# Optimization experiments

Measured on AMD Instinct MI355X. Metric: run time of the kernel, lower is better.

## Reference

```python
import jax, jax.numpy as jnp
import numpy as np

N_NODES = 50000
N_EDGES = 800000
D = 64  # node_dim == edge_dim
NEG_SLOPE = 0.2
EPS = 1e-5


def _lin_params(key, d_in, d_out):
    k1, k2 = jax.random.split(key)
    bound = 1.0 / np.sqrt(d_in)
    W = jax.random.uniform(k1, (d_out, d_in), minval=-bound, maxval=bound, dtype=jnp.float32)
    b = jax.random.uniform(k2, (d_out,), minval=-bound, maxval=bound, dtype=jnp.float32)
    return W, b


def setup_inputs() -> dict:
    key = jax.random.key(0)
    ks = jax.random.split(key, 12)
    V = jax.random.normal(ks[0], (N_NODES, D), dtype=jnp.float32)
    E = jax.random.normal(ks[1], (N_EDGES, D), dtype=jnp.float32)
    src = jax.random.randint(ks[2], (N_EDGES,), 0, N_NODES, dtype=jnp.int32)
    dst = jax.random.randint(ks[3], (N_EDGES,), 0, N_NODES, dtype=jnp.int32)
    pA_w, pA_b = _lin_params(ks[4], D, D)   # NodePooling.A
    pB_w, pB_b = _lin_params(ks[5], D, D)   # NodePooling.B
    mW1, mb1 = _lin_params(ks[6], D, D)     # edge MLP layer 1
    mW2, mb2 = _lin_params(ks[7], D, D)     # edge MLP layer 2
    BW, Bb = _lin_params(ks[8], D, D)       # GenMessage.B (scale)
    CW, Cb = _lin_params(ks[9], D, D)       # GenMessage.C (shift)
    return {"V": V, "E": E, "src": src, "dst": dst,
            "pA_w": pA_w, "pA_b": pA_b, "pB_w": pB_w, "pB_b": pB_b,
            "mW1": mW1, "mb1": mb1, "mW2": mW2, "mb2": mb2,
            "BW": BW, "Bb": Bb, "CW": CW, "Cb": Cb}


def _lrelu(x):
    return jnp.where(x >= 0, x, NEG_SLOPE * x)


def reference(V, E, src, dst, pA_w, pA_b, pB_w, pB_b, mW1, mb1, mW2, mb2, BW, Bb, CW, Cb):
    n = V.shape[0]
    # V = act(V); NodePooling: B(lrelu(A(V)))
    Va = _lrelu(V)
    Vp = _lrelu(Va @ pA_w.T + pA_b) @ pB_w.T + pB_b  # [N, D]
    # edge MLP on edge features (2 Linear+ReLU layers)
    x = jax.nn.relu(E @ mW1.T + mb1)
    x = jax.nn.relu(x @ mW2.T + mb2)                  # [E, D]
    scale = jax.nn.sigmoid(x @ BW.T + Bb)
    shift = x @ CW.T + Cb
    # gathered src features, gated affine message
    M1 = scale * Vp[src] + shift                      # [E, D]
    M2 = M1 * M1
    # segment-mean onto dst (DGL fn.mean); zero for isolated nodes
    deg = jax.ops.segment_sum(jnp.ones((dst.shape[0],), jnp.float32), dst, num_segments=n)
    denom = jnp.maximum(deg, 1.0)[:, None]
    V1 = jax.ops.segment_sum(M1, dst, num_segments=n) / denom
    V2 = jax.ops.segment_sum(M2, dst, num_segments=n) / denom
    return jnp.sqrt(jax.nn.relu(V2 - V1) + EPS)
```

## Files before the change

kernel.cpp:

```cpp
#include <hip/hip_runtime.h>

#define NN 50000
#define NE 800000
#define DDIM 64
#define PADX 68
#define PADS 68
#define NB_SCAN ((NN + 255) / 256)
#define NEG_SLOPE 0.2f
#define EPS_V 1e-5f

typedef short bf16x8 __attribute__((ext_vector_type(8)));
typedef float f32x4 __attribute__((ext_vector_type(4)));

__device__ __forceinline__ float lrelu_f(float x) { return x >= 0.0f ? x : NEG_SLOPE * x; }

__device__ __forceinline__ unsigned short bf16_rn(float x) {
    union { float f; unsigned int u; } c; c.f = x;
    unsigned int r = c.u + 0x7FFF + ((c.u >> 16) & 1);
    return (unsigned short)(r >> 16);
}
__device__ __forceinline__ float bf16_tof(unsigned short h) {
    union { float f; unsigned int u; } c; c.u = ((unsigned int)h) << 16;
    return c.f;
}

__device__ __forceinline__ unsigned cvtpk_bf16(float a, float b) {
    unsigned r;
    asm("v_cvt_pk_bf16_f32 %0, %1, %2" : "=v"(r) : "v"(a), "v"(b));
    return r;
}

__device__ __forceinline__ void split8(const float* __restrict__ v, bf16x8& h, bf16x8& l)
{
    union { bf16x8 v8; unsigned u[4]; } H, L;
    #pragma unroll
    for (int k = 0; k < 4; ++k) {
        float a = v[2*k], b = v[2*k+1];
        unsigned p = cvtpk_bf16(a, b);
        union { float f; unsigned u; } h0, h1;
        h0.u = p << 16;
        h1.u = p & 0xFFFF0000u;
        unsigned q = cvtpk_bf16(a - h0.f, b - h1.f);
        H.u[k] = p;
        L.u[k] = q;
    }
    h = H.v8; l = L.v8;
}

__device__ __forceinline__ void mma_tile(float acc[16], const float* __restrict__ XT,
                                         const float* __restrict__ Wc, int e0, int f0)
{
    #pragma unroll 4
    for (int kk = 0; kk < DDIM; kk += 4) {
        float4 A0 = *(const float4*)&XT[(kk+0)*PADX + e0];
        float4 A1 = *(const float4*)&XT[(kk+1)*PADX + e0];
        float4 A2 = *(const float4*)&XT[(kk+2)*PADX + e0];
        float4 A3 = *(const float4*)&XT[(kk+3)*PADX + e0];
        float4 B0 = *(const float4*)&Wc[(f0+0)*PADX + kk];
        float4 B1 = *(const float4*)&Wc[(f0+1)*PADX + kk];
        float4 B2 = *(const float4*)&Wc[(f0+2)*PADX + kk];
        float4 B3 = *(const float4*)&Wc[(f0+3)*PADX + kk];
        const float a[4][4] = {{A0.x,A0.y,A0.z,A0.w},{A1.x,A1.y,A1.z,A1.w},
                               {A2.x,A2.y,A2.z,A2.w},{A3.x,A3.y,A3.z,A3.w}};
        const float b[4][4] = {{B0.x,B0.y,B0.z,B0.w},{B1.x,B1.y,B1.z,B1.w},
                               {B2.x,B2.y,B2.z,B2.w},{B3.x,B3.y,B3.z,B3.w}};
        #pragma unroll
        for (int j = 0; j < 4; ++j)
            #pragma unroll
            for (int i = 0; i < 4; ++i)
                #pragma unroll
                for (int q = 0; q < 4; ++q)
                    acc[i*4+j] = fmaf(a[q][i], b[j][q], acc[i*4+j]);
    }
}

__device__ __forceinline__ void load_w_f32(float* __restrict__ Wc, const float* __restrict__ Wg, int tid)
{
    #pragma unroll
    for (int c = 0; c < 4; ++c) {
        int idx = (c << 10) + (tid << 2);
        int f = idx >> 6, k = idx & 63;
        *(float4*)&Wc[f*PADX + k] = *(const float4*)&Wg[idx];
    }
}

__global__ __launch_bounds__(256, 3)
void node_pool_kernel(const float* __restrict__ V,
                      const float* __restrict__ Aw, const float* __restrict__ Ab,
                      const float* __restrict__ Bw, const float* __restrict__ Bbv,
                      float* __restrict__ Vp,
                      const int* __restrict__ dst, int* __restrict__ degi)
{
    __shared__ float Wc[DDIM*PADX];
    __shared__ float XT[DDIM*PADX];
    const int tid = threadIdx.x;
    const int nb = blockIdx.x * 64;
    const int e0 = (tid & 15) << 2;
    const int f0 = (tid >> 4) << 2;

    #pragma unroll
    for (int c = 0; c < 4; ++c) {
        int idx = (c << 10) + (tid << 2);
        int e = idx >> 6, d = idx & 63;
        int row = nb + e; if (row > NN-1) row = NN-1;
        float4 v = *(const float4*)&V[(size_t)row*DDIM + d];
        XT[(d+0)*PADX + e] = lrelu_f(v.x);
        XT[(d+1)*PADX + e] = lrelu_f(v.y);
        XT[(d+2)*PADX + e] = lrelu_f(v.z);
        XT[(d+3)*PADX + e] = lrelu_f(v.w);
    }
    load_w_f32(Wc, Aw, tid);
    __syncthreads();

    float acc[16];
    #pragma unroll
    for (int i = 0; i < 16; ++i) acc[i] = 0.f;
    mma_tile(acc, XT, Wc, e0, f0);
    __syncthreads();

    {
        float4 bv = *(const float4*)&Ab[f0];
        const float ba[4] = {bv.x, bv.y, bv.z, bv.w};
        #pragma unroll
        for (int j = 0; j < 4; ++j) {
            float4 v;
            v.x = lrelu_f(acc[0*4+j] + ba[j]);
            v.y = lrelu_f(acc[1*4+j] + ba[j]);
            v.z = lrelu_f(acc[2*4+j] + ba[j]);
            v.w = lrelu_f(acc[3*4+j] + ba[j]);
            *(float4*)&XT[(f0+j)*PADX + e0] = v;
        }
    }
    load_w_f32(Wc, Bw, tid);
    __syncthreads();

    float acc2[16];
    #pragma unroll
    for (int i = 0; i < 16; ++i) acc2[i] = 0.f;
    mma_tile(acc2, XT, Wc, e0, f0);

    float4 bv = *(const float4*)&Bbv[f0];
    #pragma unroll
    for (int i = 0; i < 4; ++i) {
        int row = nb + e0 + i;
        if (row < NN) {
            float4 o;
            o.x = acc2[i*4+0] + bv.x;
            o.y = acc2[i*4+1] + bv.y;
            o.z = acc2[i*4+2] + bv.z;
            o.w = acc2[i*4+3] + bv.w;
            *(float4*)&Vp[(size_t)row*DDIM + f0] = o;
        }
    }

    const int stride = gridDim.x * 256;
    for (int e = blockIdx.x * 256 + tid; e < NE; e += stride)
        atomicAdd(&degi[dst[e]], 1);
}

__global__ __launch_bounds__(256)
void prep_w_kernel(const float* __restrict__ W1, const float* __restrict__ W2,
                   const float* __restrict__ WB, const float* __restrict__ WC,
                   short* __restrict__ WF)
{
    int gid = blockIdx.x * 256 + threadIdx.x;
    int L = gid >> 12, r = gid & 4095;
    int t = r >> 10, ks = (r >> 9) & 1, lane = (r >> 3) & 63, j = r & 7;
    const float* Ws = (L == 0) ? W1 : (L == 1) ? W2 : (L == 2) ? WB : WC;
    int n = lane & 15, kg = lane >> 4;
    int f = t*16 + n, k = ks*32 + kg*8 + j;
    float v = Ws[f*64 + k];
    unsigned short h = bf16_rn(v);
    unsigned short l = bf16_rn(v - bf16_tof(h));
    int base = L*8192 + ((t*2 + ks)*2)*512 + lane*8 + j;
    WF[base]       = (short)h;
    WF[base + 512] = (short)l;
}

__global__ __launch_bounds__(256)
void scan1_kernel(const int* __restrict__ degi, int* __restrict__ linc, int* __restrict__ bsum)
{
    __shared__ int ws[4];
    const int tid = threadIdx.x;
    const int lane = tid & 63, wv = tid >> 6;
    int i = blockIdx.x * 256 + tid;
    int v = (i < NN) ? degi[i] : 0;
    int sc = v;
    #pragma unroll
    for (int off = 1; off < 64; off <<= 1) {
        int t = __shfl_up(sc, off, 64);
        if (lane >= off) sc += t;
    }
    if (lane == 63) ws[wv] = sc;
    __syncthreads();
    int wb = 0;
    #pragma unroll
    for (int w = 0; w < 4; ++w) if (w < wv) wb += ws[w];
    int incl = sc + wb;
    if (i < NN) linc[i] = incl;
    if (tid == 255) bsum[blockIdx.x] = incl;
}

__global__ __launch_bounds__(256)
void scan23_kernel(const int* __restrict__ degi, const int* __restrict__ linc,
                   const int* __restrict__ bsum, int* __restrict__ curs)
{
    __shared__ int ws[4];
    __shared__ int base_s;
    const int tid = threadIdx.x;
    const int lane = tid & 63, wv = tid >> 6;
    int v = (tid < NB_SCAN) ? bsum[tid] : 0;
    int sc = v;
    #pragma unroll
    for (int off = 1; off < 64; off <<= 1) {
        int t = __shfl_up(sc, off, 64);
        if (lane >= off) sc += t;
    }
    if (lane == 63) ws[wv] = sc;
    __syncthreads();
    int wb = 0;
    #pragma unroll
    for (int w = 0; w < 4; ++w) if (w < wv) wb += ws[w];
    if (tid == blockIdx.x) base_s = sc + wb - v;
    __syncthreads();
    int i = blockIdx.x * 256 + tid;
    if (i < NN) curs[i] = base_s + linc[i] - degi[i];
}

__global__ __launch_bounds__(256)
void scatter_kernel(const int* __restrict__ dst, int* __restrict__ cursor, int* __restrict__ pinv)
{
    int e = blockIdx.x * 256 + threadIdx.x;
    if (e < NE) {
        pinv[e] = atomicAdd(&cursor[dst[e]], 1);
    }
}

__device__ __forceinline__ void gemm64_dual_lds(const short* bw, int lane,
                                                const bf16x8 ah0[2], const bf16x8 al0[2],
                                                const bf16x8 ah1[2], const bf16x8 al1[2],
                                                f32x4 acc0[4], f32x4 acc1[4])
{
    #pragma unroll
    for (int ks = 0; ks < 2; ++ks) {
        bf16x8 bh[4], bl[4];
        #pragma unroll
        for (int t = 0; t < 4; ++t) {
            bh[t] = *(const bf16x8*)&bw[(((t*2 + ks)*2 + 0)*64 + lane)*8];
            bl[t] = *(const bf16x8*)&bw[(((t*2 + ks)*2 + 1)*64 + lane)*8];
        }
        #pragma unroll
        for (int t = 0; t < 4; ++t) {
            acc0[t] = __builtin_amdgcn_mfma_f32_16x16x32_bf16(al0[ks], bh[t], acc0[t], 0, 0, 0);
            acc1[t] = __builtin_amdgcn_mfma_f32_16x16x32_bf16(al1[ks], bh[t], acc1[t], 0, 0, 0);
            acc0[t] = __builtin_amdgcn_mfma_f32_16x16x32_bf16(ah0[ks], bl[t], acc0[t], 0, 0, 0);
            acc1[t] = __builtin_amdgcn_mfma_f32_16x16x32_bf16(ah1[ks], bl[t], acc1[t], 0, 0, 0);
            acc0[t] = __builtin_amdgcn_mfma_f32_16x16x32_bf16(ah0[ks], bh[t], acc0[t], 0, 0, 0);
            acc1[t] = __builtin_amdgcn_mfma_f32_16x16x32_bf16(ah1[ks], bh[t], acc1[t], 0, 0, 0);
        }
    }
}

__device__ __forceinline__ void transpose_frags(float* __restrict__ sw, const f32x4 y[4],
                                                int lane, bf16x8 ah[2], bf16x8 al[2])
{
    const int n = lane & 15, mg = lane >> 4;
    #pragma unroll
    for (int t = 0; t < 4; ++t)
        #pragma unroll
        for (int r = 0; r < 4; ++r)
            sw[(mg*4 + r)*PADS + t*16 + n] = y[t][r];
    __builtin_amdgcn_wave_barrier();
    const int m = lane & 15, kg = lane >> 4;
    float x[16];
    *(float4*)&x[0]  = *(const float4*)&sw[m*PADS + kg*8];
    *(float4*)&x[4]  = *(const float4*)&sw[m*PADS + kg*8 + 4];
    *(float4*)&x[8]  = *(const float4*)&sw[m*PADS + 32 + kg*8];
    *(float4*)&x[12] = *(const float4*)&sw[m*PADS + 32 + kg*8 + 4];
    split8(&x[0], ah[0], al[0]);
    split8(&x[8], ah[1], al[1]);
    __builtin_amdgcn_wave_barrier();
}

__global__ __launch_bounds__(256, 3)
void e1_mlp_kernel(const float* __restrict__ Eg,
                   const int* __restrict__ src, const int* __restrict__ pinv,
                   const short* __restrict__ WF,
                   const float* __restrict__ b1, const float* __restrict__ b2,
                   const float* __restrict__ bB, const float* __restrict__ bC,
                   const float* __restrict__ Vp,
                   float* __restrict__ M1s)
{
    __shared__ short bw[8192];
    __shared__ float scratch[4 * 16 * PADS];
    __shared__ int aux[4 * 64];

    const int tid = threadIdx.x;
    const int lane = tid & 63, wv = tid >> 6;
    float* sw = scratch + wv * 16 * PADS;
    int* auxw = aux + wv * 64;

    const int e0 = blockIdx.x * 128 + wv * 32;
    const int m = lane & 15, kg = lane >> 4;
    const int n = lane & 15, mg = lane >> 4;

    auto load_layer = [&](const short* Wg) {
        __syncthreads();
        const uint4* s = (const uint4*)Wg;
        uint4* d = (uint4*)bw;
        #pragma unroll
        for (int c = 0; c < 4; ++c)
            d[c*256 + tid] = s[c*256 + tid];
        __syncthreads();
    };

    if (lane < 32) {
        auxw[lane]      = pinv[e0 + lane];
        auxw[32 + lane] = src[e0 + lane];
    }
    bf16x8 ah0[2], al0[2], ah1[2], al1[2];
    {
        const float* er0 = Eg + (size_t)(e0 + m)*DDIM + kg*8;
        const float* er1 = Eg + (size_t)(e0 + 16 + m)*DDIM + kg*8;
        float x[16];
        *(float4*)&x[0]  = *(const float4*)&er0[0];
        *(float4*)&x[4]  = *(const float4*)&er0[4];
        *(float4*)&x[8]  = *(const float4*)&er0[32];
        *(float4*)&x[12] = *(const float4*)&er0[36];
        split8(&x[0], ah0[0], al0[0]);
        split8(&x[8], ah0[1], al0[1]);
        *(float4*)&x[0]  = *(const float4*)&er1[0];
        *(float4*)&x[4]  = *(const float4*)&er1[4];
        *(float4*)&x[8]  = *(const float4*)&er1[32];
        *(float4*)&x[12] = *(const float4*)&er1[36];
        split8(&x[0], ah1[0], al1[0]);
        split8(&x[8], ah1[1], al1[1]);
    }

    load_layer(WF);
    f32x4 acc0[4], acc1[4];
    #pragma unroll
    for (int t = 0; t < 4; ++t) { acc0[t] = (f32x4){0.f,0.f,0.f,0.f}; acc1[t] = (f32x4){0.f,0.f,0.f,0.f}; }
    gemm64_dual_lds(bw, lane, ah0, al0, ah1, al1, acc0, acc1);
    #pragma unroll
    for (int t = 0; t < 4; ++t) {
        float b = b1[t*16 + n];
        #pragma unroll
        for (int r = 0; r < 4; ++r) {
            acc0[t][r] = fmaxf(acc0[t][r] + b, 0.0f);
            acc1[t][r] = fmaxf(acc1[t][r] + b, 0.0f);
        }
    }
    transpose_frags(sw, acc0, lane, ah0, al0);
    transpose_frags(sw, acc1, lane, ah1, al1);

    load_layer(WF + 8192);
    #pragma unroll
    for (int t = 0; t < 4; ++t) { acc0[t] = (f32x4){0.f,0.f,0.f,0.f}; acc1[t] = (f32x4){0.f,0.f,0.f,0.f}; }
    gemm64_dual_lds(bw, lane, ah0, al0, ah1, al1, acc0, acc1);
    #pragma unroll
    for (int t = 0; t < 4; ++t) {
        float b = b2[t*16 + n];
        #pragma unroll
        for (int r = 0; r < 4; ++r) {
            acc0[t][r] = fmaxf(acc0[t][r] + b, 0.0f);
            acc1[t][r] = fmaxf(acc1[t][r] + b, 0.0f);
        }
    }
    transpose_frags(sw, acc0, lane, ah0, al0);
    transpose_frags(sw, acc1, lane, ah1, al1);

    f32x4 accS0[4], accS1[4];
    load_layer(WF + 2*8192);
    #pragma unroll
    for (int t = 0; t < 4; ++t) { accS0[t] = (f32x4){0.f,0.f,0.f,0.f}; accS1[t] = (f32x4){0.f,0.f,0.f,0.f}; }
    gemm64_dual_lds(bw, lane, ah0, al0, ah1, al1, accS0, accS1);

    f32x4 accH0[4], accH1[4];
    load_layer(WF + 3*8192);
    #pragma unroll
    for (int t = 0; t < 4; ++t) { accH0[t] = (f32x4){0.f,0.f,0.f,0.f}; accH1[t] = (f32x4){0.f,0.f,0.f,0.f}; }
    gemm64_dual_lds(bw, lane, ah0, al0, ah1, al1, accH0, accH1);

    #pragma unroll
    for (int tile = 0; tile < 2; ++tile) {
        const int to = tile * 16;
        f32x4* accS = tile ? accS1 : accS0;
        f32x4* accH = tile ? accH1 : accH0;

        {
            int sn[4];
            #pragma unroll
            for (int r = 0; r < 4; ++r) sn[r] = auxw[32 + to + mg*4 + r];
            #pragma unroll
            for (int t = 0; t < 4; ++t) {
                const int ff = t*16 + n;
                const float bBv = bB[ff];
                const float bCv = bC[ff];
                #pragma unroll
                for (int r = 0; r < 4; ++r) {
                    float vp = Vp[(size_t)sn[r]*DDIM + ff];
                    float sg = 1.0f / (1.0f + __expf(-(accS[t][r] + bBv)));
                    sw[(mg*4 + r)*PADS + ff] = fmaf(sg, vp, accH[t][r] + bCv);
                }
            }
        }
        __builtin_amdgcn_wave_barrier();

        #pragma unroll 4
        for (int r = 0; r < 16; ++r) {
            int p = auxw[to + r];
            M1s[(size_t)p*DDIM + lane] = sw[r*PADS + lane];
        }
        __builtin_amdgcn_wave_barrier();
    }
}

__global__ __launch_bounds__(256)
void e2_reduce_kernel(const float* __restrict__ M1s,
                      const int* __restrict__ cend, const int* __restrict__ degi,
                      float* __restrict__ out)
{
    const int nw = blockIdx.x * 4 + (threadIdx.x >> 6);
    if (nw >= NN) return;
    const int lane = threadIdx.x & 63;
    const int deg = degi[nw];
    const int start = cend[nw] - deg;
    const float* base = M1s + (size_t)start*DDIM + lane;
    float s1 = 0.f, s2 = 0.f;
    int i = 0;
    for (; i + 4 <= deg; i += 4) {
        float a = base[(size_t)(i+0)*DDIM];
        float b = base[(size_t)(i+1)*DDIM];
        float c = base[(size_t)(i+2)*DDIM];
        float d = base[(size_t)(i+3)*DDIM];
        s1 += a + b + c + d;
        s2 = fmaf(a, a, s2); s2 = fmaf(b, b, s2);
        s2 = fmaf(c, c, s2); s2 = fmaf(d, d, s2);
    }
    for (; i < deg; ++i) {
        float a = base[(size_t)i*DDIM];
        s1 += a;
        s2 = fmaf(a, a, s2);
    }
    float dn = deg > 1 ? (float)deg : 1.0f;
    float v = (s2 - s1) / dn;
    out[(size_t)nw*DDIM + lane] = sqrtf(fmaxf(v, 0.0f) + EPS_V);
}

extern "C" void kernel_launch(void* const* d_in, const int* in_sizes, int n_in,
                              void* d_out, int out_size, void* d_ws, size_t ws_size,
                              hipStream_t stream) {
    const float* V   = (const float*)d_in[0];
    const float* Eg  = (const float*)d_in[1];
    const int*   src = (const int*)d_in[2];
    const int*   dst = (const int*)d_in[3];
    const float* pAw = (const float*)d_in[4];
    const float* pAb = (const float*)d_in[5];
    const float* pBw = (const float*)d_in[6];
    const float* pBb = (const float*)d_in[7];
    const float* mW1 = (const float*)d_in[8];
    const float* mb1 = (const float*)d_in[9];
    const float* mW2 = (const float*)d_in[10];
    const float* mb2 = (const float*)d_in[11];
    const float* BW  = (const float*)d_in[12];
    const float* Bb  = (const float*)d_in[13];
    const float* CW  = (const float*)d_in[14];
    const float* Cb  = (const float*)d_in[15];
    float* out = (float*)d_out;

    float* ws    = (float*)d_ws;
    float* Vp    = ws;
    int*   degi  = (int*)(ws + (size_t)NN*DDIM);
    int*   curs  = degi + NN;
    int*   linc  = curs + NN;
    int*   bsum  = linc + NN;
    int*   pinv  = bsum + NB_SCAN;
    short* WF    = (short*)(pinv + NE);
    float* M1s   = (float*)(WF + 4*8192);

    hipMemsetAsync(degi, 0, (size_t)NN * sizeof(int), stream);

    prep_w_kernel<<<64, 256, 0, stream>>>(mW1, mW2, BW, CW, WF);
    node_pool_kernel<<<(NN + 63)/64, 256, 0, stream>>>(V, pAw, pAb, pBw, pBb, Vp, dst, degi);
    scan1_kernel<<<NB_SCAN, 256, 0, stream>>>(degi, linc, bsum);
    scan23_kernel<<<NB_SCAN, 256, 0, stream>>>(degi, linc, bsum, curs);
    scatter_kernel<<<(NE + 255)/256, 256, 0, stream>>>(dst, curs, pinv);
    e1_mlp_kernel<<<NE/128, 256, 0, stream>>>(Eg, src, pinv, WF,
                                              mb1, mb2, Bb, Cb, Vp, M1s);
    e2_reduce_kernel<<<(NN + 3)/4, 256, 0, stream>>>(M1s, curs, degi, out);
}
```

Before: 535.1 us.

## Fuse segment reduction into edge MLP via dst-sorted edges and run-length atomics

Edges are processed in dst-sorted order through an index list built by the scatter kernel, so each wave sees runs of the same destination. It accumulates M1 and M1^2 per run and flushes them with float atomics into S1/S2. This removes the 205 MB M1s intermediate write and read and the separate reduce pass. In exchange, E rows are gathered by index rather than streamed, a larger memset is needed, and float atomics make the summation order nondeterministic.

Measured after the change: 505.8 us. -5.5%, faster.

```diff
diff --git a/kernel.cpp b/kernel.cpp
--- a/kernel.cpp
+++ b/kernel.cpp
@@ -228,11 +228,12 @@
 }
 
 __global__ __launch_bounds__(256)
-void scatter_kernel(const int* __restrict__ dst, int* __restrict__ cursor, int* __restrict__ pinv)
+void scatter_kernel(const int* __restrict__ dst, int* __restrict__ cursor, int* __restrict__ eidx)
 {
     int e = blockIdx.x * 256 + threadIdx.x;
     if (e < NE) {
-        pinv[e] = atomicAdd(&cursor[dst[e]], 1);
+        int p = atomicAdd(&cursor[dst[e]], 1);
+        eidx[p] = e;
     }
 }
 
@@ -283,13 +284,14 @@
 }
 
 __global__ __launch_bounds__(256, 3)
-void e1_mlp_kernel(const float* __restrict__ Eg,
-                   const int* __restrict__ src, const int* __restrict__ pinv,
-                   const short* __restrict__ WF,
-                   const float* __restrict__ b1, const float* __restrict__ b2,
-                   const float* __restrict__ bB, const float* __restrict__ bC,
-                   const float* __restrict__ Vp,
-                   float* __restrict__ M1s)
+void edge_fused_kernel(const float* __restrict__ Eg,
+                       const int* __restrict__ src, const int* __restrict__ dst,
+                       const int* __restrict__ eidx,
+                       const short* __restrict__ WF,
+                       const float* __restrict__ b1, const float* __restrict__ b2,
+                       const float* __restrict__ bB, const float* __restrict__ bC,
+                       const float* __restrict__ Vp,
+                       float* __restrict__ S1, float* __restrict__ S2)
 {
     __shared__ short bw[8192];
     __shared__ float scratch[4 * 16 * PADS];
@@ -300,7 +302,7 @@
     float* sw = scratch + wv * 16 * PADS;
     int* auxw = aux + wv * 64;
 
-    const int e0 = blockIdx.x * 128 + wv * 32;
+    const int ew = blockIdx.x * 128 + wv * 32;
     const int m = lane & 15, kg = lane >> 4;
     const int n = lane & 15, mg = lane >> 4;
 
@@ -315,13 +317,16 @@
     };
 
     if (lane < 32) {
-        auxw[lane]      = pinv[e0 + lane];
-        auxw[32 + lane] = src[e0 + lane];
+        int eg = eidx[ew + lane];
+        auxw[lane]      = src[eg];
+        auxw[32 + lane] = dst[eg];
     }
     bf16x8 ah0[2], al0[2], ah1[2], al1[2];
     {
-        const float* er0 = Eg + (size_t)(e0 + m)*DDIM + kg*8;
-        const float* er1 = Eg + (size_t)(e0 + 16 + m)*DDIM + kg*8;
+        int eg0 = eidx[ew + m];
+        int eg1 = eidx[ew + 16 + m];
+        const float* er0 = Eg + (size_t)eg0*DDIM + kg*8;
+        const float* er1 = Eg + (size_t)eg1*DDIM + kg*8;
         float x[16];
         *(float4*)&x[0]  = *(const float4*)&er0[0];
         *(float4*)&x[4]  = *(const float4*)&er0[4];
@@ -382,6 +387,9 @@
     for (int t = 0; t < 4; ++t) { accH0[t] = (f32x4){0.f,0.f,0.f,0.f}; accH1[t] = (f32x4){0.f,0.f,0.f,0.f}; }
     gemm64_dual_lds(bw, lane, ah0, al0, ah1, al1, accH0, accH1);
 
+    const int f = lane;
+    float s1 = 0.f, s2 = 0.f;
+    int prev = auxw[32];
     #pragma unroll
     for (int tile = 0; tile < 2; ++tile) {
         const int to = tile * 16;
@@ -391,7 +399,7 @@
         {
             int sn[4];
             #pragma unroll
-            for (int r = 0; r < 4; ++r) sn[r] = auxw[32 + to + mg*4 + r];
+            for (int r = 0; r < 4; ++r) sn[r] = auxw[to + mg*4 + r];
             #pragma unroll
             for (int t = 0; t < 4; ++t) {
                 const int ff = t*16 + n;
@@ -408,44 +416,34 @@
         __builtin_amdgcn_wave_barrier();
 
         #pragma unroll 4
-        for (int r = 0; r < 16; ++r) {
-            int p = auxw[to + r];
-            M1s[(size_t)p*DDIM + lane] = sw[r*PADS + lane];
+        for (int e = 0; e < 16; ++e) {
+            int dn = auxw[32 + to + e];
+            float m1 = sw[e*PADS + f];
+            float m2 = m1 * m1;
+            if (dn != prev) {
+                atomicAdd(&S1[(size_t)prev*DDIM + f], s1);
+                atomicAdd(&S2[(size_t)prev*DDIM + f], s2);
+                s1 = 0.f; s2 = 0.f; prev = dn;
+            }
+            s1 += m1; s2 += m2;
         }
         __builtin_amdgcn_wave_barrier();
     }
+    atomicAdd(&S1[(size_t)prev*DDIM + f], s1);
+    atomicAdd(&S2[(size_t)prev*DDIM + f], s2);
 }
 
 __global__ __launch_bounds__(256)
-void e2_reduce_kernel(const float* __restrict__ M1s,
-                      const int* __restrict__ cend, const int* __restrict__ degi,
-                      float* __restrict__ out)
-{
-    const int nw = blockIdx.x * 4 + (threadIdx.x >> 6);
-    if (nw >= NN) return;
-    const int lane = threadIdx.x & 63;
-    const int deg = degi[nw];
-    const int start = cend[nw] - deg;
-    const float* base = M1s + (size_t)start*DDIM + lane;
-    float s1 = 0.f, s2 = 0.f;
-    int i = 0;
-    for (; i + 4 <= deg; i += 4) {
-        float a = base[(size_t)(i+0)*DDIM];
-        float b = base[(size_t)(i+1)*DDIM];
-        float c = base[(size_t)(i+2)*DDIM];
-        float d = base[(size_t)(i+3)*DDIM];
-        s1 += a + b + c + d;
-        s2 = fmaf(a, a, s2); s2 = fmaf(b, b, s2);
-        s2 = fmaf(c, c, s2); s2 = fmaf(d, d, s2);
-    }
-    for (; i < deg; ++i) {
-        float a = base[(size_t)i*DDIM];
-        s1 += a;
-        s2 = fmaf(a, a, s2);
-    }
-    float dn = deg > 1 ? (float)deg : 1.0f;
-    float v = (s2 - s1) / dn;
-    out[(size_t)nw*DDIM + lane] = sqrtf(fmaxf(v, 0.0f) + EPS_V);
+void finalize_kernel(const float* __restrict__ S1, const float* __restrict__ S2,
+                     const int* __restrict__ degi, float* __restrict__ out)
+{
+    int gid = blockIdx.x * blockDim.x + threadIdx.x;
+    if (gid >= NN*DDIM) return;
+    int n = gid >> 6;
+    float dn = (float)degi[n];
+    dn = dn > 1.0f ? dn : 1.0f;
+    float v = (S2[gid] - S1[gid]) / dn;
+    out[gid] = sqrtf(fmaxf(v, 0.0f) + EPS_V);
 }
 
 extern "C" void kernel_launch(void* const* d_in, const int* in_sizes, int n_in,
@@ -471,22 +469,23 @@
 
     float* ws    = (float*)d_ws;
     float* Vp    = ws;
-    int*   degi  = (int*)(ws + (size_t)NN*DDIM);
+    float* S1    = ws + (size_t)NN*DDIM;
+    float* S2    = ws + (size_t)2*NN*DDIM;
+    int*   degi  = (int*)(ws + (size_t)3*NN*DDIM);
     int*   curs  = degi + NN;
     int*   linc  = curs + NN;
     int*   bsum  = linc + NN;
-    int*   pinv  = bsum + NB_SCAN;
-    short* WF    = (short*)(pinv + NE);
-    float* M1s   = (float*)(WF + 4*8192);
-
-    hipMemsetAsync(degi, 0, (size_t)NN * sizeof(int), stream);
+    int*   eidx  = bsum + NB_SCAN;
+    short* WF    = (short*)(eidx + NE);
+
+    hipMemsetAsync(S1, 0, (size_t)(2*NN*DDIM + NN) * sizeof(float), stream);
 
     prep_w_kernel<<<64, 256, 0, stream>>>(mW1, mW2, BW, CW, WF);
     node_pool_kernel<<<(NN + 63)/64, 256, 0, stream>>>(V, pAw, pAb, pBw, pBb, Vp, dst, degi);
     scan1_kernel<<<NB_SCAN, 256, 0, stream>>>(degi, linc, bsum);
     scan23_kernel<<<NB_SCAN, 256, 0, stream>>>(degi, linc, bsum, curs);
-    scatter_kernel<<<(NE + 255)/256, 256, 0, stream>>>(dst, curs, pinv);
-    e1_mlp_kernel<<<NE/128, 256, 0, stream>>>(Eg, src, pinv, WF,
-                                              mb1, mb2, Bb, Cb, Vp, M1s);
-    e2_reduce_kernel<<<(NN + 3)/4, 256, 0, stream>>>(M1s, curs, degi, out);
-}
+    scatter_kernel<<<(NE + 255)/256, 256, 0, stream>>>(dst, curs, eidx);
+    edge_fused_kernel<<<NE/128, 256, 0, stream>>>(Eg, src, dst, eidx, WF,
+                                                  mb1, mb2, Bb, Cb, Vp, S1, S2);
+    finalize_kernel<<<(NN*DDIM + 255)/256, 256, 0, stream>>>(S1, S2, degi, out);
+}
```
